# Kernel optimization log

Measured on AMD Instinct MI355X. Metric: run time of the kernel, lower is better.

The kernel has to match this reference:

```python
import jax, jax.numpy as jnp
import numpy as np
from jax import lax

EPS = 1e-12  # torch F.normalize eps
DN = ('NCHW', 'OIHW', 'NCHW')


def setup_inputs() -> dict:
    B, C, H, W, K = 16, 64, 192, 192, 3
    key = jax.random.key(0)
    k1, k2, k3 = jax.random.split(key, 3)
    x = jax.random.normal(k1, (B, C, H, W), dtype=jnp.float32)
    # Conv2d(n_feat, 2*n_feat, 3, stride=3, bias=False) weight
    w_qk = jax.random.normal(k2, (2 * C, C, 3, 3), dtype=jnp.float32) * np.float32(np.sqrt(1.0 / (C * 9)))
    # Parameter(C,C,K,K), kaiming_normal_ (fan_in=C*K*K, gain=sqrt(2)) then *0.1
    std = np.float32(np.sqrt(2.0 / (C * K * K)) * 0.1)
    weight = jax.random.normal(k3, (C, C, K, K), dtype=jnp.float32) * std
    # temperature Parameter (1,1,1); init zeros in the module, use 0.5 so the
    # dynamic-kernel branch is exercised numerically
    temperature = jnp.full((1, 1, 1), 0.5, dtype=jnp.float32)
    return {"x": x, "w_qk": w_qk, "weight": weight, "temperature": temperature}


def _l2_normalize_per_sample(t):
    # t: (B, ...) -> L2-normalize flattened per sample (torch F.normalize)
    n = jnp.sqrt(jnp.sum(t.reshape(t.shape[0], -1) ** 2, axis=-1))
    n = jnp.maximum(n, EPS).reshape((t.shape[0],) + (1,) * (t.ndim - 1))
    return t / n


def reference(x, w_qk, weight, temperature):
    B, C, H, W = x.shape
    K = weight.shape[-1]
    S = 2 * K - 1  # 5: number of spatial shifts in the cross-covariance
    P = K - 1

    # qk conv: stride-3 valid conv -> (B, 2C, H2, W2)
    qk = lax.conv_general_dilated(x, w_qk, (3, 3), 'VALID', dimension_numbers=DN)
    q, k = jnp.split(qk, 2, axis=1)
    q = _l2_normalize_per_sample(q)
    k = _l2_normalize_per_sample(k)
    H2, W2 = q.shape[2], q.shape[3]

    # cal_xtx: attn[b, co, ci, i, j] = sum_{h,w} q_pad[b, ci, i+h, j+w] * k[b, co, h, w]
    q_pad = jnp.pad(q, ((0, 0), (0, 0), (P, P), (P, P)))
    rows = []
    for i in range(S):  # fixed small 5x5 shift set
        row = []
        for j in range(S):
            sl = lax.dynamic_slice(q_pad, (0, 0, i, j), (B, C, H2, W2))
            row.append(jnp.einsum('bchw,bdhw->bdc', sl, k))  # (B, co, ci)
        rows.append(jnp.stack(row, axis=-1))
    attn = jnp.stack(rows, axis=-2)  # (B, C, C, S, S)

    # conv2d(attn.view(B*C, C, S, S), weight) valid -> (B*C, C, K, K)
    ak = lax.conv_general_dilated(attn.reshape(B * C, C, S, S), weight, (1, 1), 'VALID', dimension_numbers=DN)
    ak = ak.reshape(B, C, C, K, K).transpose(0, 2, 1, 3, 4)  # swap the two C dims

    # normalize each (C,K,K) slice per (b, c0)
    n = jnp.sqrt(jnp.sum(ak.reshape(B, C, -1) ** 2, axis=-1))
    ak = ak / jnp.maximum(n, EPS)[:, :, None, None, None]

    kern = weight[None] + ak * temperature  # (B, C, C, K, K)

    # sample-wise conv2d: groups=B trick
    out = lax.conv_general_dilated(
        x.reshape(1, B * C, H, W), kern.reshape(B * C, C, K, K), (1, 1),
        [(K // 2, K // 2)] * 2, dimension_numbers=DN, feature_group_count=B)
    return jax.nn.relu(out.reshape(B, C, H, W))
```

## Files before the change

kernel.cpp:

```cpp
#include <hip/hip_runtime.h>
#include <cstddef>

#define BB 16
#define CC_ 64
#define HH 192
#define WW 192
#define HW2 4096
#define XPH 194
#define XPW 196

typedef _Float16 f16x8 __attribute__((ext_vector_type(8)));
typedef float f32x4 __attribute__((ext_vector_type(4)));

__global__ __launch_bounds__(1024) void k_wpack(const float* __restrict__ wqk,
                                                _Float16* __restrict__ wh) {
  int e = blockIdx.x * 1024 + threadIdx.x;
  int co = e / 576, t = e % 576;
  int ci = t / 9, rs = t % 9;
  int r = rs / 3, s = rs % 3;
  int ch = ci >> 5, t32 = ci & 31;
  wh[(((r * 2 + ch) * 128 + co) * 96) + s * 32 + t32] = (_Float16)wqk[e];
}

__global__ __launch_bounds__(256) void k_xhalo(_Float16* __restrict__ xh) {
  int e = blockIdx.x * 256 + threadIdx.x;
  int b = e / 9280, i = e % 9280;
  int r, px, c;
  if (i < 3136) {
    r = (i < 1568) ? 0 : 193;
    int j = (i < 1568) ? i : i - 1568;
    px = j >> 3;
    c = j & 7;
  } else {
    int i2 = i - 3136;
    r = 1 + (i2 >> 5);
    int rem = i2 & 31;
    int sel = rem >> 3;
    px = (sel == 0) ? 0 : 192 + sel;
    c = rem & 7;
  }
  *(f16x8*)(xh + (((size_t)b * XPH + r) * XPW + px) * 64 + c * 8) =
      (f16x8)(_Float16)0;
}

__global__ __launch_bounds__(256) void k_xpack(const float* __restrict__ x,
                                               _Float16* __restrict__ xh) {
  int blk = blockIdx.x;
  int xg = blk % 3;
  int t = blk / 3;
  int y = t % 192, b = t / 192;
  int x0 = xg * 64;
  __shared__ _Float16 tl[64 * 72];
  int tid = threadIdx.x;
  int ci = tid >> 2, c4 = (tid & 3) * 16;
  const float* xp = x + ((size_t)(b * 64 + ci) * HH + y) * WW + x0 + c4;
#pragma unroll
  for (int i = 0; i < 4; ++i) {
    float4 v = *(const float4*)(xp + i * 4);
    tl[(c4 + i * 4 + 0) * 72 + ci] = (_Float16)v.x;
    tl[(c4 + i * 4 + 1) * 72 + ci] = (_Float16)v.y;
    tl[(c4 + i * 4 + 2) * 72 + ci] = (_Float16)v.z;
    tl[(c4 + i * 4 + 3) * 72 + ci] = (_Float16)v.w;
  }
  __syncthreads();
#pragma unroll
  for (int i = 0; i < 2; ++i) {
    int e = tid + 256 * i;
    int col = e >> 3, g = e & 7;
    *(f16x8*)(xh + (((size_t)b * XPH + y + 1) * XPW + x0 + 1 + col) * 64 + g * 8) =
        *(f16x8*)&tl[col * 72 + g * 8];
  }
}

__global__ __launch_bounds__(256) void k_qkconv(const _Float16* __restrict__ xh,
                                                const _Float16* __restrict__ wh,
                                                _Float16* __restrict__ qkh) {
  int blk = blockIdx.x;
  int pt = blk & 31, b = blk >> 5;
  int tid = threadIdx.x;
  int w = tid >> 6, lane = tid & 63, n16 = lane & 15, quad = lane >> 4;
  int mh = w & 1, nh = w >> 1;
  const _Float16* xb = xh + (size_t)b * (XPH * XPW * 64);

  f32x4 acc[4][4];
#pragma unroll
  for (int mt = 0; mt < 4; ++mt)
#pragma unroll
    for (int nt = 0; nt < 4; ++nt) acc[mt][nt] = (f32x4){0.f, 0.f, 0.f, 0.f};

#pragma unroll
  for (int kc = 0; kc < 6; ++kc) {
    int r = kc >> 1, ch = kc & 1;
    int irow = 6 * pt + 3 * nh + r;
    const _Float16* wp = wh + (size_t)kc * (128 * 96);
#pragma unroll
    for (int s = 0; s < 3; ++s) {
      f16x8 af[4], bf[4];
#pragma unroll
      for (int mt = 0; mt < 4; ++mt)
        af[mt] = *(const f16x8*)(wp + (mh * 64 + mt * 16 + n16) * 96 + s * 32 +
                                 quad * 8);
#pragma unroll
      for (int nt = 0; nt < 4; ++nt) {
        int col = 3 * (nt * 16 + n16) + s;
        bf[nt] = *(const f16x8*)(xb + ((size_t)(irow + 1) * XPW + col + 1) * 64 +
                                 ch * 32 + quad * 8);
      }
#pragma unroll
      for (int mt = 0; mt < 4; ++mt)
#pragma unroll
        for (int nt = 0; nt < 4; ++nt)
          acc[mt][nt] = __builtin_amdgcn_mfma_f32_16x16x32_f16(af[mt], bf[nt],
                                                               acc[mt][nt], 0, 0, 0);
    }
  }
  int py = pt * 2 + nh;
#pragma unroll
  for (int mt = 0; mt < 4; ++mt)
#pragma unroll
    for (int reg = 0; reg < 4; ++reg) {
      int co = mh * 64 + mt * 16 + quad * 4 + reg;
      _Float16* op = qkh + (size_t)(b * 128 + co) * HW2 + py * 64;
#pragma unroll
      for (int nt = 0; nt < 4; ++nt) op[nt * 16 + n16] = (_Float16)acc[mt][nt][reg];
    }
}

__global__ __launch_bounds__(256) void k_qpad(const _Float16* __restrict__ qkh,
                                              _Float16* __restrict__ qpad) {
  int blk = blockIdx.x;
  int b = blk >> 6, ci = blk & 63;
  __shared__ _Float16 qrow[4096];
  int tid = threadIdx.x;
  const _Float16* src = qkh + (size_t)(b * 128 + ci) * HW2;
#pragma unroll
  for (int i = 0; i < 2; ++i)
    ((f16x8*)qrow)[tid + 256 * i] = ((const f16x8*)src)[tid + 256 * i];
  __syncthreads();
  _Float16* dst = qpad + ((size_t)(b * 5) * 64 + ci) * 4352;
  const f16x8 zero = (f16x8)(_Float16)0;
  for (int it = tid; it < 544; it += 256) {
    int w8 = it & 7, hr = it >> 3;
    int h = hr - 2;
    bool rowok = (unsigned)h < 64u;
    f16x8 vm = (rowok && w8 > 0) ? *(const f16x8*)&qrow[h * 64 + w8 * 8 - 8] : zero;
    f16x8 vc = rowok ? *(const f16x8*)&qrow[h * 64 + w8 * 8] : zero;
    f16x8 vp = (rowok && w8 < 7) ? *(const f16x8*)&qrow[h * 64 + w8 * 8 + 8] : zero;
#pragma unroll
    for (int djx = 0; djx < 5; ++djx) {
      const int s = djx - 2;
      f16x8 r;
#pragma unroll
      for (int j = 0; j < 8; ++j) {
        const int rel = j + s;
        r[j] = (rel < 0) ? vm[8 + rel] : ((rel < 8) ? vc[rel] : vp[rel - 8]);
      }
      *(f16x8*)(dst + (size_t)djx * (64 * 4352) + hr * 64 + w8 * 8) = r;
    }
  }
}

__global__ __launch_bounds__(256) void k_attn(const _Float16* __restrict__ qkh,
                                              const _Float16* __restrict__ qpad,
                                              float* __restrict__ attn_p) {
  int blk = blockIdx.x;
  int xcd = blk & 7, j = blk >> 3;
  int b = xcd + ((j >= 50) ? 8 : 0);
  int t = (j >= 50) ? (j - 50) : j;
  int sh = t >> 1, sp = t & 1;
  int djx = sh % 5, dix = sh / 5;
  const _Float16* kb = qkh + (size_t)(b * 128 + 64) * HW2;
  const _Float16* qpb = qpad + ((size_t)(b * 5 + djx) * 64) * 4352 + dix * 64;
  int tid = threadIdx.x, w = tid >> 6, lane = tid & 63;
  int n16 = lane & 15, quad = lane >> 4;

  __shared__ float racc[64 * 66];
  for (int e = tid; e < 64 * 66; e += 256) racc[e] = 0.f;
  __syncthreads();

  f32x4 acc[4][4];
#pragma unroll
  for (int mt = 0; mt < 4; ++mt)
#pragma unroll
    for (int nt = 0; nt < 4; ++nt) acc[mt][nt] = (f32x4){0.f, 0.f, 0.f, 0.f};

  int base = sp * 2048 + w * 512 + quad * 8;
#pragma unroll 4
  for (int ks = 0; ks < 16; ++ks) {
    int p0 = base + ks * 32;
    f16x8 af[4], bf[4];
#pragma unroll
    for (int mt = 0; mt < 4; ++mt)
      af[mt] = *(const f16x8*)(kb + (size_t)(mt * 16 + n16) * HW2 + p0);
#pragma unroll
    for (int nt = 0; nt < 4; ++nt)
      bf[nt] = *(const f16x8*)(qpb + (size_t)(nt * 16 + n16) * 4352 + p0);
#pragma unroll
    for (int mt = 0; mt < 4; ++mt)
#pragma unroll
      for (int nt = 0; nt < 4; ++nt)
        acc[mt][nt] = __builtin_amdgcn_mfma_f32_16x16x32_f16(af[mt], bf[nt],
                                                             acc[mt][nt], 0, 0, 0);
  }

#pragma unroll
  for (int mt = 0; mt < 4; ++mt) {
    int co = mt * 16 + quad * 4;
#pragma unroll
    for (int reg = 0; reg < 4; ++reg)
#pragma unroll
      for (int nt = 0; nt < 4; ++nt)
        atomicAdd(&racc[(co + reg) * 66 + nt * 16 + n16], acc[mt][nt][reg]);
  }
  __syncthreads();
  float* op = attn_p + (size_t)(b * 25 + sh) * 4096;
  for (int e = tid; e < 4096; e += 256)
    atomicAdd(&op[e], racc[(e >> 6) * 66 + (e & 63)]);
}

__global__ __launch_bounds__(576) void k_akconv(const float* __restrict__ attn_p,
                                                const float* __restrict__ wgt,
                                                float* __restrict__ akt) {
  int blk = blockIdx.x;
  int b = blk >> 6, co = blk & 63;
  __shared__ float sa[64 * 25];
  int tid = threadIdx.x;
  for (int e = tid; e < 1600; e += 576) {
    int didj = e >> 6, ci = e & 63;
    size_t idx = (((size_t)b * 25 + didj) * 64 + co) * 64 + ci;
    sa[ci * 25 + didj] = attn_p[idx];
  }
  __syncthreads();
  int o = tid / 9, rs = tid % 9;
  int ki = rs / 3, kj = rs % 3;
  float acc = 0.f;
  for (int ci = 0; ci < 64; ++ci) {
    const float* wp = wgt + (o * 64 + ci) * 9;
    const float* ap = sa + ci * 25 + ki * 5 + kj;
#pragma unroll
    for (int r = 0; r < 3; ++r)
#pragma unroll
      for (int s = 0; s < 3; ++s) acc += ap[r * 5 + s] * wp[r * 3 + s];
  }
  akt[((size_t)(b * 64 + o) * 64 + co) * 9 + rs] = acc;
}

__global__ __launch_bounds__(576) void k_kern(const float* __restrict__ akt,
                                              const float* __restrict__ wgt,
                                              const float* __restrict__ temp,
                                              _Float16* __restrict__ kh) {
  int blk = blockIdx.x;
  int o = blk & 63;
  int tid = threadIdx.x;
  float v = akt[(size_t)blk * 576 + tid];
  float sq = v * v;
#pragma unroll
  for (int m = 1; m < 64; m <<= 1) sq += __shfl_xor(sq, m, 64);
  __shared__ float wsum[9];
  if ((tid & 63) == 0) wsum[tid >> 6] = sq;
  __syncthreads();
  float tot = 0.f;
#pragma unroll
  for (int i = 0; i < 9; ++i) tot += wsum[i];
  float inv = temp[0] / fmaxf(sqrtf(tot), 1e-12f);
  float kv = wgt[o * 576 + tid] + v * inv;
  int b = blk >> 6;
  int ci = tid / 9, rs = tid % 9;
  kh[(((size_t)(b * 9 + rs) * 64 + o) * 64) + ci] = (_Float16)kv;
}

__global__ __launch_bounds__(256, 3) void k_final(const _Float16* __restrict__ xh,
                                                  const _Float16* __restrict__ kh,
                                                  float* __restrict__ out) {
  int blk = blockIdx.x;
  int xt = blk % 3;
  int t2 = blk / 3;
  int yt = t2 % 48, b = t2 / 48;
  int y0 = yt * 4, x0 = xt * 64;

  __shared__ __align__(16) _Float16 xs[6 * 68 * 64];

  int tid = threadIdx.x;
  int w = tid >> 6, lane = tid & 63;
  int n16 = lane & 15, quad = lane >> 4;

  const _Float16* xb = xh + (size_t)b * (XPH * XPW * 64);
  const _Float16* kb = kh + (size_t)b * (9 * 64 * 64);

  {
    f16x8 v[13];
#pragma unroll
    for (int i = 0; i < 13; ++i) {
      int e = tid + 256 * i;
      if (e < 3264) {
        int row = e / 544, rem = e % 544;
        int px = rem >> 3, c = rem & 7;
        v[i] = *(const f16x8*)(xb + ((size_t)(y0 + row) * XPW + x0 + px) * 64 +
                               c * 8);
      }
    }
#pragma unroll
    for (int i = 0; i < 13; ++i) {
      int e = tid + 256 * i;
      if (e < 3264) {
        int row = e / 544, rem = e % 544;
        int px = rem >> 3, c = rem & 7;
        *(f16x8*)&xs[((row * 68 + px) * 8 + (c ^ (px & 7))) * 8] = v[i];
      }
    }
  }
  __syncthreads();

  f32x4 acc[4][4];
#pragma unroll
  for (int mt = 0; mt < 4; ++mt)
#pragma unroll
    for (int nt = 0; nt < 4; ++nt) acc[mt][nt] = (f32x4){0.f, 0.f, 0.f, 0.f};

#define LDAF(dst, ch_)                                                          \
  {                                                                             \
    const int rs_ = (ch_) >> 1, hi_ = (ch_)&1;                                  \
    _Pragma("unroll") for (int mt = 0; mt < 4; ++mt) dst[mt] =                  \
        *(const f16x8*)(kb + ((size_t)rs_ * 64 + mt * 16 + n16) * 64 +          \
                        hi_ * 32 + quad * 8);                                   \
  }

  f16x8 af[3][4];
  LDAF(af[0], 0)
  LDAF(af[1], 1)

#pragma unroll
  for (int ch = 0; ch < 18; ++ch) {
    if (ch + 2 < 18) LDAF(af[(ch + 2) % 3], ch + 2)
    int rs = ch >> 1, hi = ch & 1;
    int r = rs / 3, s = rs % 3;
    int trow = w + r;
    f16x8 bf[4];
#pragma unroll
    for (int nt = 0; nt < 4; ++nt) {
      int px = nt * 16 + n16 + s;
      int c = (hi * 4 + quad) ^ (px & 7);
      bf[nt] = *(const f16x8*)&xs[((trow * 68 + px) * 8 + c) * 8];
    }
#pragma unroll
    for (int mt = 0; mt < 4; ++mt)
#pragma unroll
      for (int nt = 0; nt < 4; ++nt)
        acc[mt][nt] = __builtin_amdgcn_mfma_f32_16x16x32_f16(af[ch % 3][mt],
                                                             bf[nt], acc[mt][nt],
                                                             0, 0, 0);
  }
#undef LDAF

  int y = y0 + w;
#pragma unroll
  for (int mt = 0; mt < 4; ++mt)
#pragma unroll
    for (int reg = 0; reg < 4; ++reg) {
      int o = mt * 16 + quad * 4 + reg;
      float* op = out + (((size_t)(b * 64 + o) * HH + y) * WW + x0);
#pragma unroll
      for (int nt = 0; nt < 4; ++nt)
        op[nt * 16 + n16] = fmaxf(acc[mt][nt][reg], 0.f);
    }
}

extern "C" void kernel_launch(void* const* d_in, const int* in_sizes, int n_in,
                              void* d_out, int out_size, void* d_ws, size_t ws_size,
                              hipStream_t stream) {
  const float* x = (const float*)d_in[0];
  const float* wqk = (const float*)d_in[1];
  const float* wgt = (const float*)d_in[2];
  const float* temp = (const float*)d_in[3];
  float* out = (float*)d_out;
  char* ws = (char*)d_ws;

  _Float16* xh = (_Float16*)ws;
  _Float16* qkh = (_Float16*)(ws + 77873152);
  _Float16* qpad = (_Float16*)(ws + 94650368);
  float* attn_p = (float*)(ws + 139214848);
  _Float16* wh = (_Float16*)(ws + 139067392);
  float* akt = (float*)(ws + 94650368);
  _Float16* kh = (_Float16*)(ws + 97009664);

  hipMemsetAsync(attn_p, 0, 6553600, stream);
  k_wpack<<<dim3(72), 1024, 0, stream>>>(wqk, wh);
  k_xhalo<<<dim3(580), 256, 0, stream>>>(xh);
  k_xpack<<<dim3(9216), 256, 0, stream>>>(x, xh);
  k_qkconv<<<dim3(512), 256, 0, stream>>>(xh, wh, qkh);
  k_qpad<<<dim3(1024), 256, 0, stream>>>(qkh, qpad);
  k_attn<<<dim3(800), 256, 0, stream>>>(qkh, qpad, attn_p);
  k_akconv<<<dim3(1024), 576, 0, stream>>>(attn_p, wgt, akt);
  k_kern<<<dim3(1024), 576, 0, stream>>>(akt, wgt, temp, kh);
  k_final<<<dim3(2304), 256, 0, stream>>>(xh, kh, out);
}
```

Baseline: 602.7 us.

## Restructure attn kernel: per-wave co tiles, 4-way spatial split, prefetched loads

```diff
diff --git a/kernel.cpp b/kernel.cpp
--- a/kernel.cpp
+++ b/kernel.cpp
@@ -165,57 +165,58 @@
                                               float* __restrict__ attn_p) {
   int blk = blockIdx.x;
   int xcd = blk & 7, j = blk >> 3;
-  int b = xcd + ((j >= 50) ? 8 : 0);
-  int t = (j >= 50) ? (j - 50) : j;
-  int sh = t >> 1, sp = t & 1;
+  int b = xcd + ((j >= 100) ? 8 : 0);
+  int t = (j >= 100) ? (j - 100) : j;
+  int sh = t >> 2, sp = t & 3;
   int djx = sh % 5, dix = sh / 5;
-  const _Float16* kb = qkh + (size_t)(b * 128 + 64) * HW2;
-  const _Float16* qpb = qpad + ((size_t)(b * 5 + djx) * 64) * 4352 + dix * 64;
   int tid = threadIdx.x, w = tid >> 6, lane = tid & 63;
   int n16 = lane & 15, quad = lane >> 4;
 
-  __shared__ float racc[64 * 66];
-  for (int e = tid; e < 64 * 66; e += 256) racc[e] = 0.f;
-  __syncthreads();
-
-  f32x4 acc[4][4];
-#pragma unroll
-  for (int mt = 0; mt < 4; ++mt)
-#pragma unroll
-    for (int nt = 0; nt < 4; ++nt) acc[mt][nt] = (f32x4){0.f, 0.f, 0.f, 0.f};
-
-  int base = sp * 2048 + w * 512 + quad * 8;
-#pragma unroll 4
-  for (int ks = 0; ks < 16; ++ks) {
-    int p0 = base + ks * 32;
-    f16x8 af[4], bf[4];
-#pragma unroll
-    for (int mt = 0; mt < 4; ++mt)
-      af[mt] = *(const f16x8*)(kb + (size_t)(mt * 16 + n16) * HW2 + p0);
+  const _Float16* ka = qkh + (size_t)(b * 128 + 64 + w * 16 + n16) * HW2 +
+                       sp * 1024 + quad * 8;
+  const _Float16* qa = qpad + ((size_t)(b * 5 + djx) * 64 + n16) * 4352 +
+                       dix * 64 + sp * 1024 + quad * 8;
+
+  f32x4 acc[4];
+#pragma unroll
+  for (int nt = 0; nt < 4; ++nt) acc[nt] = (f32x4){0.f, 0.f, 0.f, 0.f};
+
+  f16x8 afA, bfA[4], afB, bfB[4];
+  afA = *(const f16x8*)ka;
+#pragma unroll
+  for (int nt = 0; nt < 4; ++nt)
+    bfA[nt] = *(const f16x8*)(qa + (size_t)nt * 69632);
+
+#pragma unroll
+  for (int ks = 0; ks < 32; ks += 2) {
+    afB = *(const f16x8*)(ka + (ks + 1) * 32);
 #pragma unroll
     for (int nt = 0; nt < 4; ++nt)
-      bf[nt] = *(const f16x8*)(qpb + (size_t)(nt * 16 + n16) * 4352 + p0);
-#pragma unroll
-    for (int mt = 0; mt < 4; ++mt)
+      bfB[nt] = *(const f16x8*)(qa + (size_t)nt * 69632 + (ks + 1) * 32);
+#pragma unroll
+    for (int nt = 0; nt < 4; ++nt)
+      acc[nt] = __builtin_amdgcn_mfma_f32_16x16x32_f16(afA, bfA[nt], acc[nt],
+                                                       0, 0, 0);
+    if (ks + 2 < 32) {
+      afA = *(const f16x8*)(ka + (ks + 2) * 32);
 #pragma unroll
       for (int nt = 0; nt < 4; ++nt)
-        acc[mt][nt] = __builtin_amdgcn_mfma_f32_16x16x32_f16(af[mt], bf[nt],
-                                                             acc[mt][nt], 0, 0, 0);
-  }
-
-#pragma unroll
-  for (int mt = 0; mt < 4; ++mt) {
-    int co = mt * 16 + quad * 4;
-#pragma unroll
-    for (int reg = 0; reg < 4; ++reg)
-#pragma unroll
-      for (int nt = 0; nt < 4; ++nt)
-        atomicAdd(&racc[(co + reg) * 66 + nt * 16 + n16], acc[mt][nt][reg]);
-  }
-  __syncthreads();
+        bfA[nt] = *(const f16x8*)(qa + (size_t)nt * 69632 + (ks + 2) * 32);
+    }
+#pragma unroll
+    for (int nt = 0; nt < 4; ++nt)
+      acc[nt] = __builtin_amdgcn_mfma_f32_16x16x32_f16(afB, bfB[nt], acc[nt],
+                                                       0, 0, 0);
+  }
+
   float* op = attn_p + (size_t)(b * 25 + sh) * 4096;
-  for (int e = tid; e < 4096; e += 256)
-    atomicAdd(&op[e], racc[(e >> 6) * 66 + (e & 63)]);
+#pragma unroll
+  for (int nt = 0; nt < 4; ++nt)
+#pragma unroll
+    for (int reg = 0; reg < 4; ++reg) {
+      int co = w * 16 + quad * 4 + reg;
+      atomicAdd(&op[co * 64 + nt * 16 + n16], acc[nt][reg]);
+    }
 }
 
 __global__ __launch_bounds__(576) void k_akconv(const float* __restrict__ attn_p,
@@ -389,7 +390,7 @@
   k_xpack<<<dim3(9216), 256, 0, stream>>>(x, xh);
   k_qkconv<<<dim3(512), 256, 0, stream>>>(xh, wh, qkh);
   k_qpad<<<dim3(1024), 256, 0, stream>>>(qkh, qpad);
-  k_attn<<<dim3(800), 256, 0, stream>>>(qkh, qpad, attn_p);
+  k_attn<<<dim3(1600), 256, 0, stream>>>(qkh, qpad, attn_p);
   k_akconv<<<dim3(1024), 576, 0, stream>>>(attn_p, wgt, akt);
   k_kern<<<dim3(1024), 576, 0, stream>>>(akt, wgt, temp, kh);
   k_final<<<dim3(2304), 256, 0, stream>>>(xh, kh, out);
```

After: 591.1 us. Within noise of the previous version (-1.9%).
